# Kernel optimization log

Hardware: AMD Instinct MI355X
Metric: run time of the kernel (lower is better)

## Reference

```python
import jax, jax.numpy as jnp
import numpy as np

N_NODES = 100000
N_EDGES = 1000000
NUM_GRAPHS = 100
EPS_BN = 1e-5
EPS_GATE = 1e-6


def _bn(x, gamma, beta):
    # BatchNorm1d in training mode: batch statistics over dim 0
    mu = jnp.mean(x, axis=0)
    var = jnp.var(x, axis=0)
    return (x - mu) * jax.lax.rsqrt(var + EPS_BN) * gamma + beta


def _gated_gcn_layer(h, e, snorm_n, snorm_e, W, b, g_h, b_h, g_e, b_e, src, dst):
    # W: [5, d, d] stacking A, B, C, D, E projections; b: [5, d]
    Ah = h @ W[0] + b[0]
    Bh = h @ W[1] + b[1]
    Ce = e @ W[2] + b[2]
    Dh = h @ W[3] + b[3]
    Eh = h @ W[4] + b[4]
    # edge update: e_ji = Dh_src + Eh_dst + Ce   [E, d]
    e_new = Dh[src] + Eh[dst] + Ce
    sigma = jax.nn.sigmoid(e_new)
    # node update: gated sum of source messages at destination nodes
    num = jax.ops.segment_sum(sigma * Bh[src], dst, num_segments=h.shape[0])
    den = jax.ops.segment_sum(sigma, dst, num_segments=h.shape[0])
    h_new = Ah + num / (den + EPS_GATE)
    # graph size normalization
    h_new = h_new * snorm_n
    e_new = e_new * snorm_e
    # batch norm + relu + residual (dropout = 0.0)
    h_new = jax.nn.relu(_bn(h_new, g_h, b_h))
    e_new = jax.nn.relu(_bn(e_new, g_e, b_e))
    return h + h_new, e + e_new


def setup_inputs() -> dict:
    key = jax.random.key(0)
    ks = jax.random.split(key, 12)
    nodes_feat = jax.random.normal(ks[0], (N_NODES, 64), jnp.float32)
    edges_feat = jax.random.normal(ks[1], (N_EDGES, 1), jnp.float32)
    snorm_n = jax.random.uniform(ks[2], (N_NODES, 1), jnp.float32)
    snorm_e = jax.random.uniform(ks[3], (N_EDGES, 1), jnp.float32)
    src = jax.random.randint(ks[4], (N_EDGES,), 0, N_NODES, jnp.int32)
    dst = jax.random.randint(ks[5], (N_EDGES,), 0, N_NODES, jnp.int32)
    node_graph_ids = jnp.sort(jax.random.randint(ks[6], (N_NODES,), 0, NUM_GRAPHS, jnp.int32))
    Wh = jax.random.normal(ks[7], (64, 70), jnp.float32) * 0.1
    bh = jnp.zeros((70,), jnp.float32)
    We = jax.random.normal(ks[8], (1, 70), jnp.float32) * 0.1
    be = jnp.zeros((70,), jnp.float32)
    W_gcn = jax.random.normal(ks[9], (3, 5, 70, 70), jnp.float32) * 0.1
    b_gcn = jnp.zeros((3, 5, 70), jnp.float32)
    bn_gamma_h = jnp.ones((3, 70), jnp.float32)
    bn_beta_h = jnp.zeros((3, 70), jnp.float32)
    bn_gamma_e = jnp.ones((3, 70), jnp.float32)
    bn_beta_e = jnp.zeros((3, 70), jnp.float32)
    return {"nodes_feat": nodes_feat, "edges_feat": edges_feat, "snorm_n": snorm_n,
            "snorm_e": snorm_e, "src": src, "dst": dst, "node_graph_ids": node_graph_ids,
            "Wh": Wh, "bh": bh, "We": We, "be": be, "W_gcn": W_gcn, "b_gcn": b_gcn,
            "bn_gamma_h": bn_gamma_h, "bn_beta_h": bn_beta_h,
            "bn_gamma_e": bn_gamma_e, "bn_beta_e": bn_beta_e}


def reference(nodes_feat, edges_feat, snorm_n, snorm_e, src, dst, node_graph_ids,
              Wh, bh, We, be, W_gcn, b_gcn, bn_gamma_h, bn_beta_h, bn_gamma_e, bn_beta_e):
    h = nodes_feat @ Wh + bh
    e = edges_feat @ We + be
    # hidden_dims = [70, 70] -> only gated_gcn_1 (params index 0) and gated_gcn_o (index 2)
    for li in (0, 2):
        h, e = _gated_gcn_layer(h, e, snorm_n, snorm_e, W_gcn[li], b_gcn[li],
                                bn_gamma_h[li], bn_beta_h[li], bn_gamma_e[li], bn_beta_e[li],
                                src, dst)
    # dgl.mean_nodes: per-graph mean of node features
    sums = jax.ops.segment_sum(h, node_graph_ids, num_segments=NUM_GRAPHS)
    counts = jax.ops.segment_sum(jnp.ones((h.shape[0],), h.dtype), node_graph_ids,
                                 num_segments=NUM_GRAPHS)
    hg = sums / jnp.maximum(counts, 1.0)[:, None]
    return hg
```

## Files before the change

### kernel.cpp

```cpp
#include <hip/hip_runtime.h>

#define NN 100000
#define NE 1000000
#define NG 100
#define DD 70
#define EL0 64
#define CH0 (9 * EL0)
#define TPW 7
#define EPW (16 * TPW)
#define EPB (10 * EPW)
#define SCB 512
#define WTS (70 * 72)

typedef __attribute__((ext_vector_type(8))) short bf16x8;
typedef __attribute__((ext_vector_type(4))) float f32x4;

__device__ __forceinline__ float sigmoidf_(float x) { return 1.f / (1.f + expf(-x)); }

__device__ __forceinline__ unsigned int rne_bf16(float x) {
    unsigned int u = __float_as_uint(x);
    return (u + 0x7FFFu + ((u >> 16) & 1u)) >> 16;
}

__device__ __forceinline__ int lower_off(const int* __restrict__ off, int e) {
    int lo = 0, hi = NN - 1;
    while (lo < hi) {
        int mid = (lo + hi) >> 1;
        if (off[mid] > e) hi = mid; else lo = mid + 1;
    }
    return lo;
}

#define DOT4(acc, vv, ww) { acc = fmaf((vv).x, (ww).x, acc); acc = fmaf((vv).y, (ww).y, acc); \
                            acc = fmaf((vv).z, (ww).z, acc); acc = fmaf((vv).w, (ww).w, acc); }

__global__ void k_trAll(const float* __restrict__ Wh, const float* __restrict__ Wg,
                        float* __restrict__ WT) {
    int m = blockIdx.y, f = blockIdx.x, k = threadIdx.x;
    const float* W;
    int K = DD;
    switch (m) {
        case 0: W = Wh; K = 64; break;
        case 1: W = Wg + 0 * 4900; break;
        case 2: W = Wg + 1 * 4900; break;
        case 3: W = Wg + 3 * 4900; break;
        case 4: W = Wg + 4 * 4900; break;
        case 5: W = Wg + 10 * 4900; break;
        case 6: W = Wg + 11 * 4900; break;
        case 7: W = Wg + 13 * 4900; break;
        default: W = Wg + 14 * 4900; break;
    }
    if (k < 72) WT[(m * 70 + f) * 72 + k] = (k < K) ? W[k * DD + f] : 0.f;
}

__global__ __launch_bounds__(640) void k_dense_r(const float* __restrict__ x, int K,
                                                 const float* __restrict__ WTm,
                                                 const float* __restrict__ bias,
                                                 float* __restrict__ out, int nrows) {
    __shared__ float sx[36 * 72];
    int t = threadIdx.x;
    int r = t / DD, f = t - r * DD;
    long rb = (long)blockIdx.x * 36;
    for (int idx = t; idx < 36 * 72; idx += 640) {
        int rr = idx / 72, kk = idx - rr * 72;
        long i = rb + rr;
        sx[idx] = (kk < K && i < nrows) ? x[i * K + kk] : 0.f;
    }
    __syncthreads();
    if (r < 9) {
        const float4* wr = (const float4*)(WTm + f * 72);
        float bb = bias[f];
        float a0 = bb, a1 = bb, a2 = bb, a3 = bb;
        const float4* s0 = (const float4*)&sx[(r) * 72];
        const float4* s1 = (const float4*)&sx[(r + 9) * 72];
        const float4* s2 = (const float4*)&sx[(r + 18) * 72];
        const float4* s3 = (const float4*)&sx[(r + 27) * 72];
#pragma unroll 1
        for (int q = 0; q < 18; q += 2) {
            float4 wA = wr[q], wB = wr[q + 1];
            float4 vA0 = s0[q], vB0 = s0[q + 1];
            DOT4(a0, vA0, wA) DOT4(a0, vB0, wB)
            float4 vA1 = s1[q], vB1 = s1[q + 1];
            DOT4(a1, vA1, wA) DOT4(a1, vB1, wB)
            float4 vA2 = s2[q], vB2 = s2[q + 1];
            DOT4(a2, vA2, wA) DOT4(a2, vB2, wB)
            float4 vA3 = s3[q], vB3 = s3[q + 1];
            DOT4(a3, vA3, wA) DOT4(a3, vB3, wB)
        }
        long i0 = rb + r, i1 = i0 + 9, i2 = i0 + 18, i3 = i0 + 27;
        if (i0 < nrows) out[i0 * DD + f] = a0;
        if (i1 < nrows) out[i1 * DD + f] = a1;
        if (i2 < nrows) out[i2 * DD + f] = a2;
        if (i3 < nrows) out[i3 * DD + f] = a3;
    }
}

__global__ void k_pre(const float* __restrict__ We, const float* __restrict__ be,
                      const float* __restrict__ Wg, const float* __restrict__ bg,
                      float* __restrict__ v1, float* __restrict__ v2) {
    int f = threadIdx.x;
    if (f < DD) {
        const float* W2 = Wg + 2 * DD * DD;
        const float* b2 = bg + 2 * DD;
        float a = 0.f, c = 0.f;
        for (int k = 0; k < DD; ++k) {
            a = fmaf(We[k], W2[k * DD + f], a);
            c = fmaf(be[k], W2[k * DD + f], c);
        }
        v1[f] = a;
        v2[f] = c + b2[f];
    }
}

__global__ void k_prep2(const float* __restrict__ v1, const float* __restrict__ v2,
                        const float* __restrict__ murs_e, const float* __restrict__ ge,
                        const float* __restrict__ bbe, const float* __restrict__ We,
                        const float* __restrict__ be, const float* __restrict__ Wg,
                        float* __restrict__ CT2, unsigned short* __restrict__ WB) {
    int t = threadIdx.x;
    if (t < 35) {
        int f0 = 2 * t, f1 = 2 * t + 1;
        float A0 = murs_e[DD + f0] * ge[f0], A1 = murs_e[DD + f1] * ge[f1];
        float* c = CT2 + t * 12;
        c[0] = v1[f0];  c[1] = v1[f1];
        c[2] = v2[f0];  c[3] = v2[f1];
        c[4] = A0;      c[5] = A1;
        c[6] = bbe[f0] - murs_e[f0] * A0;
        c[7] = bbe[f1] - murs_e[f1] * A1;
        c[8] = We[f0];  c[9] = We[f1];
        c[10] = be[f0]; c[11] = be[f1];
    }
    const float* WC2 = Wg + 12 * 4900;
    for (int idx = t; idx < 960; idx += 512) {
        int nt = idx / 192, rem = idx - nt * 192;
        int c = rem / 64, l = rem - c * 64;
        int n = nt * 16 + (l & 15);
        int kb = c * 32 + (l >> 4) * 8;
        for (int j = 0; j < 8; ++j) {
            int k = kb + j;
            unsigned short v = 0;
            if (k < 70 && n < 70) v = (unsigned short)rne_bf16(WC2[k * 70 + n]);
            WB[((nt * 3 + c) * 64 + l) * 8 + j] = v;
        }
    }
}

__global__ void k_count(const int* __restrict__ dst, int* __restrict__ off) {
    int j = blockIdx.x * 256 + threadIdx.x;
    if (j < NE) atomicAdd(&off[dst[j]], 1);
}

__global__ void k_scan_a(int* __restrict__ off, int* __restrict__ part) {
    __shared__ int s[SCB];
    int t = threadIdx.x, i = blockIdx.x * SCB + t;
    int v = (i < NN) ? off[i] : 0;
    s[t] = v;
    __syncthreads();
    for (int d = 1; d < SCB; d <<= 1) {
        int x = (t >= d) ? s[t - d] : 0;
        __syncthreads();
        s[t] += x;
        __syncthreads();
    }
    if (i < NN) off[i] = s[t] - v;
    if (t == SCB - 1) part[blockIdx.x] = s[t];
}

__global__ void k_scan_b(int* __restrict__ part, int nb) {
    __shared__ int s[256];
    int t = threadIdx.x;
    int v = (t < nb) ? part[t] : 0;
    s[t] = v;
    __syncthreads();
    for (int d = 1; d < 256; d <<= 1) {
        int x = (t >= d) ? s[t - d] : 0;
        __syncthreads();
        s[t] += x;
        __syncthreads();
    }
    if (t < nb) part[t] = s[t] - v;
}

__global__ void k_scan_c(int* __restrict__ off, const int* __restrict__ part) {
    int i = blockIdx.x * SCB + threadIdx.x;
    if (i < NN) off[i] += part[blockIdx.x];
}

__global__ void k_fill(const int* __restrict__ src, const int* __restrict__ dst,
                       const float* __restrict__ ef, const float* __restrict__ sne,
                       int* __restrict__ off, int* __restrict__ src_s,
                       float* __restrict__ ef_s, float* __restrict__ sne_s) {
    int j = blockIdx.x * 256 + threadIdx.x;
    if (j < NE) {
        int d = dst[j];
        int pos = atomicAdd(&off[d], 1);
        src_s[pos] = src[j];
        ef_s[pos] = ef[j];
        sne_s[pos] = sne[j];
    }
}

__global__ __launch_bounds__(640) void k_edge0(
    const float* __restrict__ ef_s, const float* __restrict__ sne_s,
    const int* __restrict__ src_s, const int* __restrict__ off,
    const float* __restrict__ PB, const float* __restrict__ PD,
    const float* __restrict__ PE, const float* __restrict__ v1,
    const float* __restrict__ v2, float* __restrict__ num,
    float* __restrict__ den, float* __restrict__ red) {
    int t = threadIdx.x;
    int r = t / DD, f = t - r * DD;
    bool act = (r < 9);
    float c1 = 0.f, c2 = 0.f;
    if (act) { c1 = v1[f]; c2 = v2[f]; }
    float acc_s = 0.f, acc_q = 0.f;
    int e_beg = blockIdx.x * CH0 + r * EL0;
    bool live = act && e_beg < NE;
    int n = 0;
    float pe = 0.f, accn = 0.f, accd = 0.f;
    int lim = 0;
    if (live) {
        n = lower_off(off, e_beg);
        pe = PE[(long)n * DD + f];
        lim = NE - e_beg;
        if (lim > EL0) lim = EL0;
    }
    for (int g = 0; g < lim; g += 4) {
        int m = lim - g;
        if (m > 4) m = 4;
        float pdj[4], pbj[4], efj[4], snj[4];
#pragma unroll
        for (int j = 0; j < 4; ++j) {
            if (j < m) {
                int e = e_beg + g + j;
                int s = src_s[e];
                efj[j] = ef_s[e];
                snj[j] = sne_s[e];
                pdj[j] = PD[(long)s * DD + f];
                pbj[j] = PB[(long)s * DD + f];
            }
        }
#pragma unroll
        for (int j = 0; j < 4; ++j) {
            if (j < m) {
                int e = e_beg + g + j;
                if (e >= off[n]) {
                    unsafeAtomicAdd(&num[(long)n * DD + f], accn);
                    unsafeAtomicAdd(&den[(long)n * DD + f], accd);
                    accn = 0.f; accd = 0.f;
                    do { ++n; } while (off[n] <= e);
                    pe = PE[(long)n * DD + f];
                }
                float en = pdj[j] + pe + efj[j] * c1 + c2;
                float sg = sigmoidf_(en);
                accn = fmaf(sg, pbj[j], accn);
                accd += sg;
                float tv = en * snj[j];
                acc_s += tv;
                acc_q = fmaf(tv, tv, acc_q);
            }
        }
    }
    if (live) {
        unsafeAtomicAdd(&num[(long)n * DD + f], accn);
        unsafeAtomicAdd(&den[(long)n * DD + f], accd);
    }
    __shared__ float ss[DD], sq[DD];
    if (t < DD) { ss[t] = 0.f; sq[t] = 0.f; }
    __syncthreads();
    if (act) { atomicAdd(&ss[f], acc_s); atomicAdd(&sq[f], acc_q); }
    __syncthreads();
    if (t < DD) {
        atomicAdd(&red[t], ss[t]);
        atomicAdd(&red[DD + t], sq[t]);
    }
}

__global__ __launch_bounds__(640) void k_edge2(
    const float* __restrict__ ef_s, const float* __restrict__ sne_s,
    const int* __restrict__ src_s, const int* __restrict__ off,
    const float* __restrict__ PD0, const float* __restrict__ PE0,
    const float* __restrict__ PB2, const float* __restrict__ PD2,
    const float* __restrict__ PE2, const float* __restrict__ CT2,
    const unsigned short* __restrict__ WB, const float* __restrict__ bC2,
    float* __restrict__ num, float* __restrict__ den) {
    __shared__ __align__(16) unsigned short As[10 * 16 * 104];
    int t = threadIdx.x;
    int w = t >> 6, l = t & 63;
    unsigned short* Aw = &As[w * 1664];
    for (int i = l; i < 832; i += 64) ((unsigned int*)Aw)[i] = 0u;
    int wb_e = blockIdx.x * EPB + w * EPW;
    if (wb_e >= NE) return;
    int col = l & 15, hi = l >> 4;
    bf16x8 bfr[15];
#pragma unroll
    for (int q = 0; q < 15; ++q)
        bfr[q] = *(const bf16x8*)(WB + (q * 64 + l) * 8);
    float bc[5];
#pragma unroll
    for (int nt = 0; nt < 5; ++nt) bc[nt] = bC2[nt * 16 + col];
    int e0s = wb_e + (l / 35);
    if (e0s > NE - 1) e0s = NE - 1;
    int ns = lower_off(off, e0s);
    int e0p = wb_e + hi * 4;
    if (e0p > NE - 1) e0p = NE - 1;
    int np = lower_off(off, e0p);
    float pe2c[5], an[5], ad[5];
#pragma unroll
    for (int nt = 0; nt < 5; ++nt) {
        pe2c[nt] = PE2[(long)np * DD + nt * 16 + col];
        an[nt] = 0.f; ad[nt] = 0.f;
    }
    for (int tt = 0; tt < TPW; ++tt) {
        int et = wb_e + tt * 16;
        if (et >= NE) break;
        for (int i = l; i < 560; i += 64) {
            int el = i / 35, fp = i - el * 35, f = fp * 2;
            int e = et + el;
            unsigned int val = 0u;
            if (e < NE) {
                while (off[ns] <= e) ++ns;
                int s = src_s[e];
                float efv = ef_s[e], sn = sne_s[e];
                const float* ct = CT2 + fp * 12;
                float2 pd = *(const float2*)(PD0 + (long)s * DD + f);
                float2 pe = *(const float2*)(PE0 + (long)ns * DD + f);
                float en0a = pd.x + pe.x + efv * ct[0] + ct[2];
                float en0b = pd.y + pe.y + efv * ct[1] + ct[3];
                float ra = fmaxf(fmaf(en0a * sn, ct[4], ct[6]), 0.f);
                float rb = fmaxf(fmaf(en0b * sn, ct[5], ct[7]), 0.f);
                float e1a = fmaf(efv, ct[8], ct[10]) + ra;
                float e1b = fmaf(efv, ct[9], ct[11]) + rb;
                val = rne_bf16(e1a) | (rne_bf16(e1b) << 16);
            }
            ((unsigned int*)Aw)[(el * 104 + f) >> 1] = val;
        }
        bf16x8 af[3];
#pragma unroll
        for (int c = 0; c < 3; ++c)
            af[c] = *(const bf16x8*)(Aw + (l & 15) * 104 + c * 32 + hi * 8);
        f32x4 acc[5];
#pragma unroll
        for (int nt = 0; nt < 5; ++nt) {
            acc[nt] = (f32x4){0.f, 0.f, 0.f, 0.f};
#pragma unroll
            for (int c = 0; c < 3; ++c)
                acc[nt] = __builtin_amdgcn_mfma_f32_16x16x32_bf16(af[c], bfr[nt * 3 + c],
                                                                  acc[nt], 0, 0, 0);
        }
#pragma unroll
        for (int j = 0; j < 4; ++j) {
            int e = et + hi * 4 + j;
            if (e < NE) {
                if (e >= off[np]) {
#pragma unroll
                    for (int nt = 0; nt < 5; ++nt) {
                        int nv = nt * 16 + col;
                        if (nv < 70) {
                            unsafeAtomicAdd(&num[(long)np * DD + nv], an[nt]);
                            unsafeAtomicAdd(&den[(long)np * DD + nv], ad[nt]);
                        }
                        an[nt] = 0.f; ad[nt] = 0.f;
                    }
                    do { ++np; } while (off[np] <= e);
#pragma unroll
                    for (int nt = 0; nt < 5; ++nt)
                        pe2c[nt] = PE2[(long)np * DD + nt * 16 + col];
                }
                int s = src_s[e];
#pragma unroll
                for (int nt = 0; nt < 5; ++nt) {
                    int nv = nt * 16 + col;
                    if (nv < 70) {
                        float en = acc[nt][j] + bc[nt] + PD2[(long)s * DD + nv] + pe2c[nt];
                        float sg = sigmoidf_(en);
                        an[nt] = fmaf(sg, PB2[(long)s * DD + nv], an[nt]);
                        ad[nt] += sg;
                    }
                }
            }
        }
    }
#pragma unroll
    for (int nt = 0; nt < 5; ++nt) {
        int nv = nt * 16 + col;
        if (nv < 70) {
            unsafeAtomicAdd(&num[(long)np * DD + nv], an[nt]);
            unsafeAtomicAdd(&den[(long)np * DD + nv], ad[nt]);
        }
    }
}

__global__ __launch_bounds__(640) void k_nstats(const float* __restrict__ PA,
                                                const float* __restrict__ num,
                                                const float* __restrict__ den,
                                                const float* __restrict__ snn,
                                                float* __restrict__ red) {
    int t = threadIdx.x;
    int r = t / DD, f = t - r * DD;
    bool act = (r < 9);
    float acc_s = 0.f, acc_q = 0.f;
    const int T = (NN + 8) / 9;
    for (int tile = blockIdx.x; tile < T; tile += gridDim.x) {
        int i = tile * 9 + r;
        if (act && i < NN) {
            long o = (long)i * DD + f;
            float v = (PA[o] + num[o] / (den[o] + 1e-6f)) * snn[i];
            acc_s += v;
            acc_q = fmaf(v, v, acc_q);
        }
    }
    __shared__ float ss[DD], sq[DD];
    if (t < DD) { ss[t] = 0.f; sq[t] = 0.f; }
    __syncthreads();
    if (act) { atomicAdd(&ss[f], acc_s); atomicAdd(&sq[f], acc_q); }
    __syncthreads();
    if (t < DD) {
        atomicAdd(&red[t], ss[t]);
        atomicAdd(&red[DD + t], sq[t]);
    }
}

__global__ void k_stats(const float* __restrict__ sums, float* __restrict__ murs, float invn) {
    int f = threadIdx.x;
    if (f < DD) {
        float mu = sums[f] * invn;
        float var = sums[DD + f] * invn - mu * mu;
        murs[f] = mu;
        murs[DD + f] = rsqrtf(var + 1e-5f);
    }
}

__global__ __launch_bounds__(256) void k_apply(const float* __restrict__ hin,
                                               const float* __restrict__ PA,
                                               const float* __restrict__ num,
                                               const float* __restrict__ den,
                                               const float* __restrict__ snn,
                                               const float* __restrict__ murs,
                                               const float* __restrict__ g,
                                               const float* __restrict__ b,
                                               float* __restrict__ hout) {
    long idx = (long)blockIdx.x * 256 + threadIdx.x;
    if (idx < (long)NN * DD) {
        int i = (int)(idx / DD);
        int f = (int)(idx - (long)i * DD);
        float v = (PA[idx] + num[idx] / (den[idx] + 1e-6f)) * snn[i];
        float bnv = (v - murs[f]) * murs[DD + f] * g[f] + b[f];
        hout[idx] = hin[idx] + fmaxf(bnv, 0.f);
    }
}

__global__ __launch_bounds__(640) void k_readout(const float* __restrict__ h,
                                                 const int* __restrict__ gid,
                                                 float* __restrict__ gsum,
                                                 float* __restrict__ gcnt) {
    __shared__ float sv[9 * DD];
    __shared__ int sg_[9];
    int t = threadIdx.x;
    int r = t / DD, f = t - r * DD;
    int i = blockIdx.x * 9 + r;
    if (r < 9 && i < NN) {
        sv[r * DD + f] = h[(long)i * DD + f];
        if (f == 0) sg_[r] = gid[i];
    }
    __syncthreads();
    int nvalid = NN - blockIdx.x * 9;
    if (nvalid > 9) nvalid = 9;
    if (t < DD && nvalid > 0) {
        float acc = 0.f;
        int cur = sg_[0];
        for (int rr = 0; rr < nvalid; ++rr) {
            int g = sg_[rr];
            if (g != cur) {
                unsafeAtomicAdd(&gsum[cur * DD + t], acc);
                acc = 0.f;
                cur = g;
            }
            acc += sv[rr * DD + t];
        }
        unsafeAtomicAdd(&gsum[cur * DD + t], acc);
        if (t == 0) {
            int cnt = 0;
            cur = sg_[0];
            for (int rr = 0; rr < nvalid; ++rr) {
                if (sg_[rr] != cur) {
                    unsafeAtomicAdd(&gcnt[cur], (float)cnt);
                    cnt = 0;
                    cur = sg_[rr];
                }
                cnt++;
            }
            unsafeAtomicAdd(&gcnt[cur], (float)cnt);
        }
    }
}

__global__ void k_out(const float* __restrict__ gsum, const float* __restrict__ gcnt,
                      float* __restrict__ out) {
    int idx = blockIdx.x * 256 + threadIdx.x;
    if (idx < NG * DD) {
        int g = idx / DD;
        out[idx] = gsum[idx] / fmaxf(gcnt[g], 1.f);
    }
}

extern "C" void kernel_launch(void* const* d_in, const int* in_sizes, int n_in,
                              void* d_out, int out_size, void* d_ws, size_t ws_size,
                              hipStream_t stream) {
    const float* x   = (const float*)d_in[0];
    const float* ef  = (const float*)d_in[1];
    const float* snn = (const float*)d_in[2];
    const float* sne = (const float*)d_in[3];
    const int*   src = (const int*)d_in[4];
    const int*   dst = (const int*)d_in[5];
    const int*   gid = (const int*)d_in[6];
    const float* Wh  = (const float*)d_in[7];
    const float* bh  = (const float*)d_in[8];
    const float* We  = (const float*)d_in[9];
    const float* be  = (const float*)d_in[10];
    const float* Wg  = (const float*)d_in[11];
    const float* bg  = (const float*)d_in[12];
    const float* gh  = (const float*)d_in[13];
    const float* bbh = (const float*)d_in[14];
    const float* ge  = (const float*)d_in[15];
    const float* bbe = (const float*)d_in[16];
    float* out = (float*)d_out;

    const size_t NF = (size_t)NN * DD;

    float* ws = (float*)d_ws;
    float* B0 = ws;
    float* B1 = B0 + NF;
    float* B2 = B1 + NF;
    float* B3 = B2 + NF;
    float* B4 = B3 + NF;
    float* B5 = B4 + NF;
    float* B6 = B5 + NF;
    float* num = B6 + NF;
    float* den = num + NF;
    float* red  = den + NF;
    float* gsum = red + 4 * DD;
    float* gcnt = gsum + NG * DD;
    float* v1 = gcnt + NG;
    float* v2 = v1 + DD;
    float* murs_e = v2 + DD;
    float* murs_h = murs_e + 2 * DD;
    int* off   = (int*)(murs_h + 2 * DD);
    int* part  = off + NN;
    int* src_s = part + 256;
    float* ef_s  = (float*)(src_s + NE);
    float* sne_s = ef_s + NE;
    float* WT    = sne_s + NE;
    uintptr_t pal = ((uintptr_t)(WT + 10 * WTS) + 15) & ~(uintptr_t)15;
    float* CT2 = (float*)pal;
    unsigned short* WB = (unsigned short*)(CT2 + 420);

    size_t need = (size_t)((char*)(WB + 7680) - (char*)d_ws);
    if (ws_size < need) return;

    const int NB_N36 = (NN + 35) / 36;
    const int NB_N9  = (NN + 8) / 9;
    const int NB_E256 = (NE + 255) / 256;
    const int NB_SC  = (NN + SCB - 1) / SCB;
    const int NB_E0  = (NE + CH0 - 1) / CH0;
    const int NB_E2  = (NE + EPB - 1) / EPB;

    hipMemsetAsync(num, 0, (2 * NF + 4 * DD + NG * DD + NG) * sizeof(float), stream);
    hipMemsetAsync(off, 0, NN * sizeof(int), stream);

    k_trAll<<<dim3(70, 9), 72, 0, stream>>>(Wh, Wg, WT);
    k_count<<<NB_E256, 256, 0, stream>>>(dst, off);
    k_scan_a<<<NB_SC, SCB, 0, stream>>>(off, part);
    k_scan_b<<<1, 256, 0, stream>>>(part, NB_SC);
    k_scan_c<<<NB_SC, SCB, 0, stream>>>(off, part);
    k_fill<<<NB_E256, 256, 0, stream>>>(src, dst, ef, sne, off, src_s, ef_s, sne_s);

    k_pre<<<1, 128, 0, stream>>>(We, be, Wg, bg, v1, v2);
    k_dense_r<<<NB_N36, 640, 0, stream>>>(x, 64, WT + 0 * WTS, bh, B0, NN);

    k_dense_r<<<NB_N36, 640, 0, stream>>>(B0, 70, WT + 1 * WTS, bg + 0 * 70, B2, NN);
    k_dense_r<<<NB_N36, 640, 0, stream>>>(B0, 70, WT + 2 * WTS, bg + 1 * 70, B3, NN);
    k_dense_r<<<NB_N36, 640, 0, stream>>>(B0, 70, WT + 3 * WTS, bg + 3 * 70, B4, NN);
    k_dense_r<<<NB_N36, 640, 0, stream>>>(B0, 70, WT + 4 * WTS, bg + 4 * 70, B5, NN);
    k_edge0<<<NB_E0, 640, 0, stream>>>(ef_s, sne_s, src_s, off, B3, B4, B5, v1, v2,
                                       num, den, red);
    k_stats<<<1, 128, 0, stream>>>(red, murs_e, 1.f / NE);
    k_prep2<<<1, 512, 0, stream>>>(v1, v2, murs_e, ge + 0, bbe + 0, We, be, Wg, CT2, WB);
    k_nstats<<<2048, 640, 0, stream>>>(B2, num, den, snn, red + 2 * DD);
    k_stats<<<1, 128, 0, stream>>>(red + 2 * DD, murs_h, 1.f / NN);
    k_apply<<<(int)((NF + 255) / 256), 256, 0, stream>>>(B0, B2, num, den, snn, murs_h,
                                                         gh + 0, bbh + 0, B1);

    hipMemsetAsync(num, 0, (2 * NF + 4 * DD) * sizeof(float), stream);
    k_dense_r<<<NB_N36, 640, 0, stream>>>(B1, 70, WT + 5 * WTS, bg + 10 * 70, B2, NN);
    k_dense_r<<<NB_N36, 640, 0, stream>>>(B1, 70, WT + 6 * WTS, bg + 11 * 70, B3, NN);
    k_dense_r<<<NB_N36, 640, 0, stream>>>(B1, 70, WT + 7 * WTS, bg + 13 * 70, B0, NN);
    k_dense_r<<<NB_N36, 640, 0, stream>>>(B1, 70, WT + 8 * WTS, bg + 14 * 70, B6, NN);
    k_edge2<<<NB_E2, 640, 0, stream>>>(ef_s, sne_s, src_s, off, B4, B5, B3, B0, B6,
                                       CT2, WB, bg + 12 * 70, num, den);
    k_nstats<<<2048, 640, 0, stream>>>(B2, num, den, snn, red + 2 * DD);
    k_stats<<<1, 128, 0, stream>>>(red + 2 * DD, murs_h, 1.f / NN);
    k_apply<<<(int)((NF + 255) / 256), 256, 0, stream>>>(B1, B2, num, den, snn, murs_h,
                                                         gh + 2 * DD, bbh + 2 * DD, B0);

    k_readout<<<NB_N9, 640, 0, stream>>>(B0, gid, gsum, gcnt);
    k_out<<<(NG * DD + 255) / 256, 256, 0, stream>>>(gsum, gcnt, out);
}
```

Before: 1.904 ms.

## Store sorted destination ids per edge instead of searching CSR offsets

The fill kernel now writes each edge's destination into a sorted dst array. The edge kernels read that array instead of binary-searching and walking the offsets array, and load the destination-side projection per edge rather than caching it per segment. The offsets buffer now aliases the num accumulator, with the memset of num moved after the fill, and tiles per wave in the second edge kernel drop from 7 to 5. This removes the serial search and offset-walk latency but adds an extra per-edge index load and more per-edge PE gathers.

```diff
diff --git a/kernel.cpp b/kernel.cpp
--- a/kernel.cpp
+++ b/kernel.cpp
@@ -6,7 +6,7 @@
 #define DD 70
 #define EL0 64
 #define CH0 (9 * EL0)
-#define TPW 7
+#define TPW 5
 #define EPW (16 * TPW)
 #define EPB (10 * EPW)
 #define SCB 512
@@ -20,15 +20,6 @@
 __device__ __forceinline__ unsigned int rne_bf16(float x) {
     unsigned int u = __float_as_uint(x);
     return (u + 0x7FFFu + ((u >> 16) & 1u)) >> 16;
-}
-
-__device__ __forceinline__ int lower_off(const int* __restrict__ off, int e) {
-    int lo = 0, hi = NN - 1;
-    while (lo < hi) {
-        int mid = (lo + hi) >> 1;
-        if (off[mid] > e) hi = mid; else lo = mid + 1;
-    }
-    return lo;
 }
 
 #define DOT4(acc, vv, ww) { acc = fmaf((vv).x, (ww).x, acc); acc = fmaf((vv).y, (ww).y, acc); \
@@ -189,7 +180,8 @@
 __global__ void k_fill(const int* __restrict__ src, const int* __restrict__ dst,
                        const float* __restrict__ ef, const float* __restrict__ sne,
                        int* __restrict__ off, int* __restrict__ src_s,
-                       float* __restrict__ ef_s, float* __restrict__ sne_s) {
+                       float* __restrict__ ef_s, float* __restrict__ sne_s,
+                       int* __restrict__ dst_s) {
     int j = blockIdx.x * 256 + threadIdx.x;
     if (j < NE) {
         int d = dst[j];
@@ -197,12 +189,13 @@
         src_s[pos] = src[j];
         ef_s[pos] = ef[j];
         sne_s[pos] = sne[j];
+        dst_s[pos] = d;
     }
 }
 
 __global__ __launch_bounds__(640) void k_edge0(
     const float* __restrict__ ef_s, const float* __restrict__ sne_s,
-    const int* __restrict__ src_s, const int* __restrict__ off,
+    const int* __restrict__ src_s, const int* __restrict__ dst_s,
     const float* __restrict__ PB, const float* __restrict__ PD,
     const float* __restrict__ PE, const float* __restrict__ v1,
     const float* __restrict__ v2, float* __restrict__ num,
@@ -215,42 +208,43 @@
     float acc_s = 0.f, acc_q = 0.f;
     int e_beg = blockIdx.x * CH0 + r * EL0;
     bool live = act && e_beg < NE;
-    int n = 0;
-    float pe = 0.f, accn = 0.f, accd = 0.f;
+    int dcur = 0;
+    float accn = 0.f, accd = 0.f;
     int lim = 0;
     if (live) {
-        n = lower_off(off, e_beg);
-        pe = PE[(long)n * DD + f];
+        dcur = dst_s[e_beg];
         lim = NE - e_beg;
         if (lim > EL0) lim = EL0;
     }
     for (int g = 0; g < lim; g += 4) {
         int m = lim - g;
         if (m > 4) m = 4;
-        float pdj[4], pbj[4], efj[4], snj[4];
+        int dj[4];
+        float pdj[4], pbj[4], pej[4], efj[4], snj[4];
 #pragma unroll
         for (int j = 0; j < 4; ++j) {
             if (j < m) {
                 int e = e_beg + g + j;
                 int s = src_s[e];
+                int d = dst_s[e];
+                dj[j] = d;
                 efj[j] = ef_s[e];
                 snj[j] = sne_s[e];
                 pdj[j] = PD[(long)s * DD + f];
                 pbj[j] = PB[(long)s * DD + f];
+                pej[j] = PE[(long)d * DD + f];
             }
         }
 #pragma unroll
         for (int j = 0; j < 4; ++j) {
             if (j < m) {
-                int e = e_beg + g + j;
-                if (e >= off[n]) {
-                    unsafeAtomicAdd(&num[(long)n * DD + f], accn);
-                    unsafeAtomicAdd(&den[(long)n * DD + f], accd);
+                if (dj[j] != dcur) {
+                    unsafeAtomicAdd(&num[(long)dcur * DD + f], accn);
+                    unsafeAtomicAdd(&den[(long)dcur * DD + f], accd);
                     accn = 0.f; accd = 0.f;
-                    do { ++n; } while (off[n] <= e);
-                    pe = PE[(long)n * DD + f];
+                    dcur = dj[j];
                 }
-                float en = pdj[j] + pe + efj[j] * c1 + c2;
+                float en = pdj[j] + pej[j] + efj[j] * c1 + c2;
                 float sg = sigmoidf_(en);
                 accn = fmaf(sg, pbj[j], accn);
                 accd += sg;
@@ -261,8 +255,8 @@
         }
     }
     if (live) {
-        unsafeAtomicAdd(&num[(long)n * DD + f], accn);
-        unsafeAtomicAdd(&den[(long)n * DD + f], accd);
+        unsafeAtomicAdd(&num[(long)dcur * DD + f], accn);
+        unsafeAtomicAdd(&den[(long)dcur * DD + f], accd);
     }
     __shared__ float ss[DD], sq[DD];
     if (t < DD) { ss[t] = 0.f; sq[t] = 0.f; }
@@ -277,7 +271,7 @@
 
 __global__ __launch_bounds__(640) void k_edge2(
     const float* __restrict__ ef_s, const float* __restrict__ sne_s,
-    const int* __restrict__ src_s, const int* __restrict__ off,
+    const int* __restrict__ src_s, const int* __restrict__ dst_s,
     const float* __restrict__ PD0, const float* __restrict__ PE0,
     const float* __restrict__ PB2, const float* __restrict__ PD2,
     const float* __restrict__ PE2, const float* __restrict__ CT2,
@@ -298,18 +292,12 @@
     float bc[5];
 #pragma unroll
     for (int nt = 0; nt < 5; ++nt) bc[nt] = bC2[nt * 16 + col];
-    int e0s = wb_e + (l / 35);
-    if (e0s > NE - 1) e0s = NE - 1;
-    int ns = lower_off(off, e0s);
     int e0p = wb_e + hi * 4;
     if (e0p > NE - 1) e0p = NE - 1;
-    int np = lower_off(off, e0p);
-    float pe2c[5], an[5], ad[5];
-#pragma unroll
-    for (int nt = 0; nt < 5; ++nt) {
-        pe2c[nt] = PE2[(long)np * DD + nt * 16 + col];
-        an[nt] = 0.f; ad[nt] = 0.f;
-    }
+    int dcur = dst_s[e0p];
+    float an[5], ad[5];
+#pragma unroll
+    for (int nt = 0; nt < 5; ++nt) { an[nt] = 0.f; ad[nt] = 0.f; }
     for (int tt = 0; tt < TPW; ++tt) {
         int et = wb_e + tt * 16;
         if (et >= NE) break;
@@ -318,12 +306,11 @@
             int e = et + el;
             unsigned int val = 0u;
             if (e < NE) {
-                while (off[ns] <= e) ++ns;
-                int s = src_s[e];
+                int s = src_s[e], d = dst_s[e];
                 float efv = ef_s[e], sn = sne_s[e];
                 const float* ct = CT2 + fp * 12;
                 float2 pd = *(const float2*)(PD0 + (long)s * DD + f);
-                float2 pe = *(const float2*)(PE0 + (long)ns * DD + f);
+                float2 pe = *(const float2*)(PE0 + (long)d * DD + f);
                 float en0a = pd.x + pe.x + efv * ct[0] + ct[2];
                 float en0b = pd.y + pe.y + efv * ct[1] + ct[3];
                 float ra = fmaxf(fmaf(en0a * sn, ct[4], ct[6]), 0.f);
@@ -351,27 +338,26 @@
         for (int j = 0; j < 4; ++j) {
             int e = et + hi * 4 + j;
             if (e < NE) {
-                if (e >= off[np]) {
+                int d = dst_s[e];
+                if (d != dcur) {
 #pragma unroll
                     for (int nt = 0; nt < 5; ++nt) {
                         int nv = nt * 16 + col;
                         if (nv < 70) {
-                            unsafeAtomicAdd(&num[(long)np * DD + nv], an[nt]);
-                            unsafeAtomicAdd(&den[(long)np * DD + nv], ad[nt]);
+                            unsafeAtomicAdd(&num[(long)dcur * DD + nv], an[nt]);
+                            unsafeAtomicAdd(&den[(long)dcur * DD + nv], ad[nt]);
                         }
                         an[nt] = 0.f; ad[nt] = 0.f;
                     }
-                    do { ++np; } while (off[np] <= e);
-#pragma unroll
-                    for (int nt = 0; nt < 5; ++nt)
-                        pe2c[nt] = PE2[(long)np * DD + nt * 16 + col];
+                    dcur = d;
                 }
                 int s = src_s[e];
 #pragma unroll
                 for (int nt = 0; nt < 5; ++nt) {
                     int nv = nt * 16 + col;
                     if (nv < 70) {
-                        float en = acc[nt][j] + bc[nt] + PD2[(long)s * DD + nv] + pe2c[nt];
+                        float en = acc[nt][j] + bc[nt] + PD2[(long)s * DD + nv]
+                                 + PE2[(long)d * DD + nv];
                         float sg = sigmoidf_(en);
                         an[nt] = fmaf(sg, PB2[(long)s * DD + nv], an[nt]);
                         ad[nt] += sg;
@@ -384,8 +370,8 @@
     for (int nt = 0; nt < 5; ++nt) {
         int nv = nt * 16 + col;
         if (nv < 70) {
-            unsafeAtomicAdd(&num[(long)np * DD + nv], an[nt]);
-            unsafeAtomicAdd(&den[(long)np * DD + nv], ad[nt]);
+            unsafeAtomicAdd(&num[(long)dcur * DD + nv], an[nt]);
+            unsafeAtomicAdd(&den[(long)dcur * DD + nv], ad[nt]);
         }
     }
 }
@@ -544,15 +530,16 @@
     float* v2 = v1 + DD;
     float* murs_e = v2 + DD;
     float* murs_h = murs_e + 2 * DD;
-    int* off   = (int*)(murs_h + 2 * DD);
-    int* part  = off + NN;
-    int* src_s = part + 256;
+    int* src_s = (int*)(murs_h + 2 * DD);
     float* ef_s  = (float*)(src_s + NE);
     float* sne_s = ef_s + NE;
-    float* WT    = sne_s + NE;
+    int* dst_s = (int*)(sne_s + NE);
+    float* WT    = (float*)(dst_s + NE);
     uintptr_t pal = ((uintptr_t)(WT + 10 * WTS) + 15) & ~(uintptr_t)15;
     float* CT2 = (float*)pal;
     unsigned short* WB = (unsigned short*)(CT2 + 420);
+    int* off  = (int*)num;
+    int* part = off + NN;
 
     size_t need = (size_t)((char*)(WB + 7680) - (char*)d_ws);
     if (ws_size < need) return;
@@ -564,15 +551,15 @@
     const int NB_E0  = (NE + CH0 - 1) / CH0;
     const int NB_E2  = (NE + EPB - 1) / EPB;
 
-    hipMemsetAsync(num, 0, (2 * NF + 4 * DD + NG * DD + NG) * sizeof(float), stream);
     hipMemsetAsync(off, 0, NN * sizeof(int), stream);
-
     k_trAll<<<dim3(70, 9), 72, 0, stream>>>(Wh, Wg, WT);
     k_count<<<NB_E256, 256, 0, stream>>>(dst, off);
     k_scan_a<<<NB_SC, SCB, 0, stream>>>(off, part);
     k_scan_b<<<1, 256, 0, stream>>>(part, NB_SC);
     k_scan_c<<<NB_SC, SCB, 0, stream>>>(off, part);
-    k_fill<<<NB_E256, 256, 0, stream>>>(src, dst, ef, sne, off, src_s, ef_s, sne_s);
+    k_fill<<<NB_E256, 256, 0, stream>>>(src, dst, ef, sne, off, src_s, ef_s, sne_s, dst_s);
+
+    hipMemsetAsync(num, 0, (2 * NF + 4 * DD + NG * DD + NG) * sizeof(float), stream);
 
     k_pre<<<1, 128, 0, stream>>>(We, be, Wg, bg, v1, v2);
     k_dense_r<<<NB_N36, 640, 0, stream>>>(x, 64, WT + 0 * WTS, bh, B0, NN);
@@ -581,7 +568,7 @@
     k_dense_r<<<NB_N36, 640, 0, stream>>>(B0, 70, WT + 2 * WTS, bg + 1 * 70, B3, NN);
     k_dense_r<<<NB_N36, 640, 0, stream>>>(B0, 70, WT + 3 * WTS, bg + 3 * 70, B4, NN);
     k_dense_r<<<NB_N36, 640, 0, stream>>>(B0, 70, WT + 4 * WTS, bg + 4 * 70, B5, NN);
-    k_edge0<<<NB_E0, 640, 0, stream>>>(ef_s, sne_s, src_s, off, B3, B4, B5, v1, v2,
+    k_edge0<<<NB_E0, 640, 0, stream>>>(ef_s, sne_s, src_s, dst_s, B3, B4, B5, v1, v2,
                                        num, den, red);
     k_stats<<<1, 128, 0, stream>>>(red, murs_e, 1.f / NE);
     k_prep2<<<1, 512, 0, stream>>>(v1, v2, murs_e, ge + 0, bbe + 0, We, be, Wg, CT2, WB);
@@ -595,7 +582,7 @@
     k_dense_r<<<NB_N36, 640, 0, stream>>>(B1, 70, WT + 6 * WTS, bg + 11 * 70, B3, NN);
     k_dense_r<<<NB_N36, 640, 0, stream>>>(B1, 70, WT + 7 * WTS, bg + 13 * 70, B0, NN);
     k_dense_r<<<NB_N36, 640, 0, stream>>>(B1, 70, WT + 8 * WTS, bg + 14 * 70, B6, NN);
-    k_edge2<<<NB_E2, 640, 0, stream>>>(ef_s, sne_s, src_s, off, B4, B5, B3, B0, B6,
+    k_edge2<<<NB_E2, 640, 0, stream>>>(ef_s, sne_s, src_s, dst_s, B4, B5, B3, B0, B6,
                                        CT2, WB, bg + 12 * 70, num, den);
     k_nstats<<<2048, 640, 0, stream>>>(B2, num, den, snn, red + 2 * DD);
     k_stats<<<1, 128, 0, stream>>>(red + 2 * DD, murs_h, 1.f / NN);
```

After: 1.746 ms. -8.3%, faster.
